# Kernel optimization log

Hardware: AMD Instinct MI355X
Metric: run time of the kernel (lower is better)

## Reference

```python
import jax, jax.numpy as jnp
import numpy as np

# Quantization constants from the original module
X_ZP = -66   # int8 zero point
Y_ZP = 160   # uint8 zero point


def setup_inputs() -> dict:
    key = jax.random.key(0)
    k1, k2 = jax.random.split(key)
    # x: [7, B, M, K] int8 in [-128, 127]
    x = jax.random.randint(k1, (7, 8, 512, 1024), -128, 128, dtype=jnp.int32).astype(jnp.int8)
    # y: [B, K, N] uint8 in [0, 255]
    y = jax.random.randint(k2, (8, 1024, 512), 0, 256, dtype=jnp.int32).astype(jnp.uint8)
    return {
        "x": x,
        "y": y,
        "x_scale": jnp.float32(0.03),
        "y_scale": jnp.float32(0.025),
    }


def reference(x, y, x_scale, y_scale):
    # dequantize_per_tensor: (q - zero_point) * scale
    xf = (x.astype(jnp.float32) - jnp.float32(X_ZP)) * x_scale   # [7, B, M, K]
    yf = (y.astype(jnp.float32) - jnp.float32(Y_ZP)) * y_scale   # [B, K, N]
    # torch.matmul broadcast: [7,B,M,K] @ [B,K,N] -> [7,B,M,N]
    return jnp.einsum('gbmk,bkn->gbmn', xf, yf)
```

## Files before the change

### kernel.cpp

```cpp
#include <hip/hip_runtime.h>
#include <stdint.h>

#define AS1 __attribute__((address_space(1)))
#define AS3 __attribute__((address_space(3)))

typedef int v4i __attribute__((ext_vector_type(4)));

constexpr int G = 7, B = 8, M = 512, N = 512, K = 1024;
constexpr int GBn = G * B;

constexpr size_t YT_BYTES = (size_t)B * N * K;
constexpr size_t CSP_CNT  = (size_t)16 * B * N;
constexpr size_t WS_NEEDED = YT_BYTES + CSP_CNT * 4;

__global__ __launch_bounds__(256) void transpose_pack_y(const int* __restrict__ y,
                                                        signed char* __restrict__ yt,
                                                        int* __restrict__ csp) {
    __shared__ unsigned char tile[64][80];
    int n0  = blockIdx.x * 64;
    int k0t = blockIdx.y;
    int k0  = k0t * 64;
    int b   = blockIdx.z;
    int t   = threadIdx.x;

    int r  = t >> 2;
    int c0 = (t & 3) * 16;
    const int* src = y + ((size_t)b * K + k0 + r) * N + n0 + c0;
    uint32_t p[4];
#pragma unroll
    for (int q = 0; q < 4; ++q) {
        int4 v = ((const int4*)src)[q];
        p[q] =  (uint32_t)((v.x & 255) ^ 128)
             | ((uint32_t)((v.y & 255) ^ 128) << 8)
             | ((uint32_t)((v.z & 255) ^ 128) << 16)
             | ((uint32_t)((v.w & 255) ^ 128) << 24);
    }
    *(uint4*)&tile[r][c0] = make_uint4(p[0], p[1], p[2], p[3]);
    __syncthreads();

    int nl = t >> 2;
    int kc = (t & 3) * 16;
    uint32_t q[4];
    int s = 0;
#pragma unroll
    for (int w = 0; w < 4; ++w) {
        uint32_t b0 = tile[kc + w * 4 + 0][nl];
        uint32_t b1 = tile[kc + w * 4 + 1][nl];
        uint32_t b2 = tile[kc + w * 4 + 2][nl];
        uint32_t b3 = tile[kc + w * 4 + 3][nl];
        s += (int)(signed char)b0 + (int)(signed char)b1
           + (int)(signed char)b2 + (int)(signed char)b3;
        q[w] = b0 | (b1 << 8) | (b2 << 16) | (b3 << 24);
    }
    *(uint4*)(yt + ((size_t)b * N + n0 + nl) * K + k0 + kc) = make_uint4(q[0], q[1], q[2], q[3]);

    s += __shfl_xor(s, 1, 64);
    s += __shfl_xor(s, 2, 64);
    if ((t & 3) == 0) csp[(size_t)k0t * (B * N) + b * N + n0 + nl] = s;
}

__global__ __launch_bounds__(1024, 4) void gemm_fused(const int* __restrict__ x,
                                                      const signed char* __restrict__ yt,
                                                      const int* __restrict__ csp,
                                                      const float* __restrict__ xsp,
                                                      const float* __restrict__ ysp,
                                                      float* __restrict__ out) {
    __shared__ __align__(16) signed char As[2][128 * 64];
    __shared__ __align__(16) signed char Bs[2][512 * 64];
    __shared__ int cs_lds[512];
    __shared__ int rs_lds[128];

    int id  = blockIdx.x;
    int swz = (id & 7) * 28 + (id >> 3);
    int gb  = swz >> 2;
    int mt  = swz & 3;
    int b   = gb & 7;

    int tid = threadIdx.x, wave = tid >> 6, lane = tid & 63;

    if (tid < 512) {
        int s = 0;
        const int* p = csp + b * N + tid;
#pragma unroll
        for (int kt = 0; kt < 16; ++kt) s += p[(size_t)kt * (B * N)];
        cs_lds[tid] = s;
    }

    int arow = tid >> 3;
    int a8   = tid & 7;
    const int4* Asrc = (const int4*)(x + ((size_t)(gb * M + mt * 128 + arow)) * K) + a8 * 2;
    int aoff = arow * 64 + ((((a8 >> 1) ^ ((arow >> 1) & 3))) << 4) + ((a8 & 1) << 3);

    int brl    = lane >> 2;
    int bchunk = (lane & 3) ^ ((lane >> 3) & 3);
    const signed char* Bsrc = yt + ((size_t)(b * N)) * K;

    int fr = lane & 15;
    int fk = ((lane >> 4) ^ ((fr >> 1) & 3)) << 4;
    int wm = (wave >> 3) * 64;
    int wn = (wave & 7) * 64;

    v4i zero = {0, 0, 0, 0};
    v4i acc[4][4];
#pragma unroll
    for (int i = 0; i < 4; ++i)
#pragma unroll
        for (int j = 0; j < 4; ++j) acc[i][j] = zero;

    int rsum = 0;

    int4 av0 = Asrc[0], av1 = Asrc[1];
#pragma unroll
    for (int c = 0; c < 2; ++c) {
        __builtin_amdgcn_global_load_lds(
            (const AS1 uint32_t*)(Bsrc + (size_t)(wave * 32 + c * 16 + brl) * K + bchunk * 16),
            (AS3 uint32_t*)(&Bs[0][(wave * 32 + c * 16) * 64]), 16, 0, 0);
    }

#pragma unroll 2
    for (int t = 0; t < 16; ++t) {
        int cur = t & 1;

        {
            int4 v0 = av0, v1 = av1;
            rsum += v0.x + v0.y + v0.z + v0.w + v1.x + v1.y + v1.z + v1.w;
            uint32_t lo =  (uint32_t)(v0.x & 255)
                        | ((uint32_t)(v0.y & 255) << 8)
                        | ((uint32_t)(v0.z & 255) << 16)
                        | ((uint32_t)(v0.w & 255) << 24);
            uint32_t hi =  (uint32_t)(v1.x & 255)
                        | ((uint32_t)(v1.y & 255) << 8)
                        | ((uint32_t)(v1.z & 255) << 16)
                        | ((uint32_t)(v1.w & 255) << 24);
            *(uint2*)(&As[cur][aoff]) = make_uint2(lo, hi);
        }

        __syncthreads();

        if (t < 15) {
            av0 = Asrc[(t + 1) * 16 + 0];
            av1 = Asrc[(t + 1) * 16 + 1];
#pragma unroll
            for (int c = 0; c < 2; ++c) {
                __builtin_amdgcn_global_load_lds(
                    (const AS1 uint32_t*)(Bsrc + (size_t)(wave * 32 + c * 16 + brl) * K
                                          + (t + 1) * 64 + bchunk * 16),
                    (AS3 uint32_t*)(&Bs[cur ^ 1][(wave * 32 + c * 16) * 64]), 16, 0, 0);
            }
        }

        v4i af[4], bf[4];
#pragma unroll
        for (int i = 0; i < 4; ++i)
            af[i] = *(const v4i*)(&As[cur][(wm + i * 16 + fr) * 64 + fk]);
#pragma unroll
        for (int j = 0; j < 4; ++j)
            bf[j] = *(const v4i*)(&Bs[cur][(wn + j * 16 + fr) * 64 + fk]);

#pragma unroll
        for (int i = 0; i < 4; ++i)
#pragma unroll
            for (int j = 0; j < 4; ++j)
                acc[i][j] = __builtin_amdgcn_mfma_i32_16x16x64_i8(af[i], bf[j], acc[i][j], 0, 0, 0);
    }

    rsum += __shfl_xor(rsum, 1, 64);
    rsum += __shfl_xor(rsum, 2, 64);
    rsum += __shfl_xor(rsum, 4, 64);
    if ((tid & 7) == 0) rs_lds[arow] = rsum;
    __syncthreads();

    float sc = xsp[0] * ysp[0];
    int colL = lane & 15;
    int rowQ = (lane >> 4) * 4;
    float* outg = out + (size_t)gb * (M * N) + (size_t)(mt * 128) * N;
#pragma unroll
    for (int i = 0; i < 4; ++i) {
#pragma unroll
        for (int r = 0; r < 4; ++r) {
            int row_l = wm + i * 16 + rowQ + r;
            int rsv = rs_lds[row_l];
#pragma unroll
            for (int j = 0; j < 4; ++j) {
                int col = wn + j * 16 + colL;
                int tv = acc[i][j][r] - 32 * rsv + 66 * cs_lds[col] - 2162688;
                outg[(size_t)row_l * N + col] = sc * (float)tv;
            }
        }
    }
}

__global__ __launch_bounds__(256) void naive_kernel(const int* __restrict__ x,
                                                    const int* __restrict__ y,
                                                    const float* __restrict__ xsp,
                                                    const float* __restrict__ ysp,
                                                    float* __restrict__ out) {
    size_t idx = (size_t)blockIdx.x * 256 + threadIdx.x;
    int n  = (int)(idx & 511);
    int m  = (int)((idx >> 9) & 511);
    int gb = (int)(idx >> 18);
    int b  = gb & 7;
    const int* xr = x + ((size_t)gb * M + m) * K;
    const int* yc = y + (size_t)b * K * N + n;
    int dot = 0, sx = 0, sy = 0;
    for (int k = 0; k < K; ++k) {
        int a = xr[k];
        int c = yc[(size_t)k * N];
        dot += a * c; sx += a; sy += c;
    }
    float s = xsp[0] * ysp[0];
    out[idx] = s * (float)(dot - 160 * sx + 66 * sy - 10813440);
}

extern "C" void kernel_launch(void* const* d_in, const int* in_sizes, int n_in,
                              void* d_out, int out_size, void* d_ws, size_t ws_size,
                              hipStream_t stream) {
    const int*   x  = (const int*)d_in[0];
    const int*   y  = (const int*)d_in[1];
    const float* xs = (const float*)d_in[2];
    const float* ys = (const float*)d_in[3];
    float* out = (float*)d_out;

    if (ws_size < WS_NEEDED) {
        naive_kernel<<<(14680064 + 255) / 256, 256, 0, stream>>>(x, y, xs, ys, out);
        return;
    }

    char* ws = (char*)d_ws;
    signed char* yt  = (signed char*)ws;
    int*         csp = (int*)(ws + YT_BYTES);

    transpose_pack_y<<<dim3(N / 64, K / 64, B), 256, 0, stream>>>(y, yt, csp);
    gemm_fused<<<dim3(224), 1024, 0, stream>>>(x, yt, csp, xs, ys, out);
}
```

Measured before the change: 217.7 us.

## Stage full A tile in LDS once and stream B fragments directly from global

The GEMM kernel now loads and packs the whole 128x1024 int8 A block into a 128KB LDS buffer up front, with an XOR swizzle, then runs the K loop without any barriers. B fragments are read straight from the transposed yt buffer in global memory into registers instead of being staged through LDS with double buffering. This removes the per-step __syncthreads and the LDS round trip for B. In exchange it gives up overlap between the A loads and MFMA work, and each wave fetches B from global/L2 on its own, so the same B data is read twice per block.

```diff
diff --git a/kernel.cpp b/kernel.cpp
--- a/kernel.cpp
+++ b/kernel.cpp
@@ -1,8 +1,5 @@
 #include <hip/hip_runtime.h>
 #include <stdint.h>
-
-#define AS1 __attribute__((address_space(1)))
-#define AS3 __attribute__((address_space(3)))
 
 typedef int v4i __attribute__((ext_vector_type(4)));
 
@@ -59,14 +56,13 @@
     if ((t & 3) == 0) csp[(size_t)k0t * (B * N) + b * N + n0 + nl] = s;
 }
 
-__global__ __launch_bounds__(1024, 4) void gemm_fused(const int* __restrict__ x,
-                                                      const signed char* __restrict__ yt,
-                                                      const int* __restrict__ csp,
-                                                      const float* __restrict__ xsp,
-                                                      const float* __restrict__ ysp,
-                                                      float* __restrict__ out) {
-    __shared__ __align__(16) signed char As[2][128 * 64];
-    __shared__ __align__(16) signed char Bs[2][512 * 64];
+__global__ __launch_bounds__(1024) void gemm_fused(const int* __restrict__ x,
+                                                   const signed char* __restrict__ yt,
+                                                   const int* __restrict__ csp,
+                                                   const float* __restrict__ xsp,
+                                                   const float* __restrict__ ysp,
+                                                   float* __restrict__ out) {
+    __shared__ __align__(16) signed char Ap[128 * 1024];
     __shared__ int cs_lds[512];
     __shared__ int rs_lds[128];
 
@@ -86,89 +82,70 @@
         cs_lds[tid] = s;
     }
 
-    int arow = tid >> 3;
-    int a8   = tid & 7;
-    const int4* Asrc = (const int4*)(x + ((size_t)(gb * M + mt * 128 + arow)) * K) + a8 * 2;
-    int aoff = arow * 64 + ((((a8 >> 1) ^ ((arow >> 1) & 3))) << 4) + ((a8 & 1) << 3);
-
-    int brl    = lane >> 2;
-    int bchunk = (lane & 3) ^ ((lane >> 3) & 3);
-    const signed char* Bsrc = yt + ((size_t)(b * N)) * K;
-
-    int fr = lane & 15;
-    int fk = ((lane >> 4) ^ ((fr >> 1) & 3)) << 4;
-    int wm = (wave >> 3) * 64;
-    int wn = (wave & 7) * 64;
-
-    v4i zero = {0, 0, 0, 0};
-    v4i acc[4][4];
-#pragma unroll
-    for (int i = 0; i < 4; ++i)
-#pragma unroll
-        for (int j = 0; j < 4; ++j) acc[i][j] = zero;
-
+    int r  = tid >> 3;
+    int a8 = tid & 7;
+    const int4* Arow = (const int4*)(x + ((size_t)(gb * M + mt * 128 + r)) * K);
     int rsum = 0;
-
-    int4 av0 = Asrc[0], av1 = Asrc[1];
-#pragma unroll
-    for (int c = 0; c < 2; ++c) {
-        __builtin_amdgcn_global_load_lds(
-            (const AS1 uint32_t*)(Bsrc + (size_t)(wave * 32 + c * 16 + brl) * K + bchunk * 16),
-            (AS3 uint32_t*)(&Bs[0][(wave * 32 + c * 16) * 64]), 16, 0, 0);
-    }
-
-#pragma unroll 2
-    for (int t = 0; t < 16; ++t) {
-        int cur = t & 1;
-
-        {
-            int4 v0 = av0, v1 = av1;
-            rsum += v0.x + v0.y + v0.z + v0.w + v1.x + v1.y + v1.z + v1.w;
-            uint32_t lo =  (uint32_t)(v0.x & 255)
-                        | ((uint32_t)(v0.y & 255) << 8)
-                        | ((uint32_t)(v0.z & 255) << 16)
-                        | ((uint32_t)(v0.w & 255) << 24);
-            uint32_t hi =  (uint32_t)(v1.x & 255)
-                        | ((uint32_t)(v1.y & 255) << 8)
-                        | ((uint32_t)(v1.z & 255) << 16)
-                        | ((uint32_t)(v1.w & 255) << 24);
-            *(uint2*)(&As[cur][aoff]) = make_uint2(lo, hi);
+#pragma unroll
+    for (int ii = 0; ii < 4; ++ii) {
+        int4 v[8];
+#pragma unroll
+        for (int u = 0; u < 8; ++u) v[u] = Arow[a8 + 8 * (ii * 8 + u)];
+#pragma unroll
+        for (int u = 0; u < 8; ++u) {
+            int i = ii * 8 + u;
+            int4 t = v[u];
+            rsum += t.x + t.y + t.z + t.w;
+            uint32_t w =  (uint32_t)(t.x & 255)
+                       | ((uint32_t)(t.y & 255) << 8)
+                       | ((uint32_t)(t.z & 255) << 16)
+                       | ((uint32_t)(t.w & 255) << 24);
+            int c = (a8 >> 2) + 2 * i;
+            *(uint32_t*)(&Ap[r * 1024 + ((c ^ (r & 7)) << 4) + ((a8 & 3) << 2)]) = w;
         }
-
-        __syncthreads();
-
-        if (t < 15) {
-            av0 = Asrc[(t + 1) * 16 + 0];
-            av1 = Asrc[(t + 1) * 16 + 1];
-#pragma unroll
-            for (int c = 0; c < 2; ++c) {
-                __builtin_amdgcn_global_load_lds(
-                    (const AS1 uint32_t*)(Bsrc + (size_t)(wave * 32 + c * 16 + brl) * K
-                                          + (t + 1) * 64 + bchunk * 16),
-                    (AS3 uint32_t*)(&Bs[cur ^ 1][(wave * 32 + c * 16) * 64]), 16, 0, 0);
-            }
-        }
-
-        v4i af[4], bf[4];
-#pragma unroll
-        for (int i = 0; i < 4; ++i)
-            af[i] = *(const v4i*)(&As[cur][(wm + i * 16 + fr) * 64 + fk]);
-#pragma unroll
-        for (int j = 0; j < 4; ++j)
-            bf[j] = *(const v4i*)(&Bs[cur][(wn + j * 16 + fr) * 64 + fk]);
-
-#pragma unroll
-        for (int i = 0; i < 4; ++i)
-#pragma unroll
-            for (int j = 0; j < 4; ++j)
-                acc[i][j] = __builtin_amdgcn_mfma_i32_16x16x64_i8(af[i], bf[j], acc[i][j], 0, 0, 0);
-    }
-
+    }
     rsum += __shfl_xor(rsum, 1, 64);
     rsum += __shfl_xor(rsum, 2, 64);
     rsum += __shfl_xor(rsum, 4, 64);
-    if ((tid & 7) == 0) rs_lds[arow] = rsum;
+    if ((tid & 7) == 0) rs_lds[r] = rsum;
+
     __syncthreads();
+
+    int fr = lane & 15;
+    int h  = lane >> 4;
+    int s3 = fr & 7;
+    int wm = (wave >> 3) * 64;
+    int wn = (wave & 7) * 64;
+
+    int arow0 = (wm + fr) * 1024;
+    int aeven = arow0 + (((h)      ^ s3) << 4);
+    int aodd  = arow0 + (((4 + h)  ^ s3) << 4);
+
+    const signed char* Bj0 = yt + ((size_t)(b * N + wn + fr)) * K + h * 16;
+
+    v4i zero = {0, 0, 0, 0};
+    v4i acc[4][4];
+#pragma unroll
+    for (int i = 0; i < 4; ++i)
+#pragma unroll
+        for (int j = 0; j < 4; ++j) acc[i][j] = zero;
+
+#pragma unroll
+    for (int t = 0; t < 16; ++t) {
+        v4i bf[4], af[4];
+#pragma unroll
+        for (int j = 0; j < 4; ++j)
+            bf[j] = *(const v4i*)(Bj0 + (size_t)j * 16 * K + t * 64);
+        int ab = (t & 1) ? aodd : aeven;
+#pragma unroll
+        for (int i = 0; i < 4; ++i)
+            af[i] = *(const v4i*)(&Ap[ab + i * 16384 + (t >> 1) * 128]);
+#pragma unroll
+        for (int i = 0; i < 4; ++i)
+#pragma unroll
+            for (int j = 0; j < 4; ++j)
+                acc[i][j] = __builtin_amdgcn_mfma_i32_16x16x64_i8(af[i], bf[j], acc[i][j], 0, 0, 0);
+    }
 
     float sc = xsp[0] * ysp[0];
     int colL = lane & 15;
@@ -177,13 +154,13 @@
 #pragma unroll
     for (int i = 0; i < 4; ++i) {
 #pragma unroll
-        for (int r = 0; r < 4; ++r) {
-            int row_l = wm + i * 16 + rowQ + r;
+        for (int rr = 0; rr < 4; ++rr) {
+            int row_l = wm + i * 16 + rowQ + rr;
             int rsv = rs_lds[row_l];
 #pragma unroll
             for (int j = 0; j < 4; ++j) {
                 int col = wn + j * 16 + colL;
-                int tv = acc[i][j][r] - 32 * rsv + 66 * cs_lds[col] - 2162688;
+                int tv = acc[i][j][rr] - 32 * rsv + 66 * cs_lds[col] - 2162688;
                 outg[(size_t)row_l * N + col] = sc * (float)tv;
             }
         }
```

After: 230.5 us. 1.06x slower.
